# Optimization experiments

Measured on AMD Instinct MI355X. Metric: run time of the kernel, lower is better.

## Reference

```python
import jax, jax.numpy as jnp
import numpy as np

I_DIM = 512   # encoder feature size fed to CfC
UNITS = 1024  # AutoNCP total units (hidden_dim)
OUT = 128     # motor neurons (output_dim)
N = [538, 358, 128]                      # inter, command, motor layer sizes
IN_TOT = [I_DIM + N[0], N[0] + N[1], N[1] + N[2]]  # concat(input, h) width per layer
B, T = 512, 128


def setup_inputs() -> dict:
    key = jax.random.key(0)
    ks = jax.random.split(key, 40)
    d = {}
    d["x"] = jax.random.normal(ks[0], (B, T, I_DIM), jnp.float32)
    d["h0"] = jnp.zeros((B, UNITS), jnp.float32)
    ki = 1
    for l in range(3):
        it, n = IN_TOT[l], N[l]
        sp = (jax.random.uniform(ks[ki], (n, it - n)) < 0.5).astype(jnp.float32); ki += 1
        d[f"mask{l}"] = jnp.concatenate([sp, jnp.ones((n, n), jnp.float32)], axis=1)
        for name in ("Wff1", "Wff2", "Wta", "Wtb"):
            d[f"{name}_{l}"] = jax.random.normal(ks[ki], (n, it), jnp.float32) * float(1.0 / np.sqrt(it)); ki += 1
        for name in ("bff1", "bff2", "bta", "btb"):
            d[f"{name}_{l}"] = jnp.zeros((n,), jnp.float32)
    d["Wfc"] = jax.random.normal(ks[ki], (OUT, OUT), jnp.float32) * float(1.0 / np.sqrt(OUT))
    d["bfc"] = jnp.zeros((OUT,), jnp.float32)
    return d


def _cell(xin, h, p):
    # CfCCell, mode='default', no backbone, ts = 1.0
    W1, b1, W2, b2, Wa, ba, Wb, bb = p
    xc = jnp.concatenate([xin, h], axis=-1)           # (B, in+n)
    ff1 = jnp.tanh(xc @ W1.T + b1)
    ff2 = jnp.tanh(xc @ W2.T + b2)
    t_interp = jax.nn.sigmoid((xc @ Wa.T + ba) + (xc @ Wb.T + bb))
    return ff1 * (1.0 - t_interp) + t_interp * ff2


def reference(x, h0, mask0, Wff1_0, Wff2_0, Wta_0, Wtb_0, bff1_0, bff2_0, bta_0, btb_0,
              mask1, Wff1_1, Wff2_1, Wta_1, Wtb_1, bff1_1, bff2_1, bta_1, btb_1,
              mask2, Wff1_2, Wff2_2, Wta_2, Wtb_2, bff1_2, bff2_2, bta_2, btb_2,
              Wfc, bfc):
    params = (
        (Wff1_0 * mask0, bff1_0, Wff2_0 * mask0, bff2_0, Wta_0, bta_0, Wtb_0, btb_0),
        (Wff1_1 * mask1, bff1_1, Wff2_1 * mask1, bff2_1, Wta_1, bta_1, Wtb_1, btb_1),
        (Wff1_2 * mask2, bff1_2, Wff2_2 * mask2, bff2_2, Wta_2, bta_2, Wtb_2, btb_2),
    )
    hs0 = tuple(jnp.split(h0, [N[0], N[0] + N[1]], axis=1))

    def step(hs, x_t):
        inp = x_t
        new = []
        for l in range(3):
            inp = _cell(inp, hs[l], params[l])
            new.append(inp)
        return tuple(new), inp  # last layer (motor) is the cell output

    carry, outs = jax.lax.scan(step, hs0, jnp.swapaxes(x, 0, 1))
    outputs = jnp.swapaxes(outs, 0, 1)        # (B, T, OUT)
    hn = jnp.concatenate(carry, axis=1)       # (B, UNITS)
    predictions = outputs @ Wfc.T + bfc       # final nn.Linear
    return predictions, hn
```

## Files before the change

kernel.cpp:

```cpp
#include <hip/hip_runtime.h>
#include <stdint.h>

typedef __attribute__((ext_vector_type(8))) short short8;
typedef __attribute__((ext_vector_type(4))) float float4v;
typedef __attribute__((ext_vector_type(4))) unsigned short ushort4v;

constexpr int T = 128;
constexpr int NB = 512;
constexpr int NCH = 16;
constexpr int CBLK = 12;
constexpr int HS = 1056;

__device__ __forceinline__ float bf2f(ushort u) {
  union { float f; uint32_t i; } v; v.i = ((uint32_t)u) << 16; return v.f;
}
__device__ __forceinline__ ushort f2bf(float f) {
  union { float f; uint32_t i; } v; v.f = f;
  uint32_t i = v.i;
  uint32_t r = i + 0x7FFFu + ((i >> 16) & 1u);
  return (ushort)(r >> 16);
}

__device__ __forceinline__ unsigned long long coh_load8(const float* p) {
  return __hip_atomic_load(
      reinterpret_cast<unsigned long long*>(const_cast<float*>(p)),
      __ATOMIC_RELAXED, __HIP_MEMORY_SCOPE_AGENT);
}
__device__ __forceinline__ void coh_store8(float* p, float a, float b) {
  union { unsigned long long u; float f[2]; } v; v.f[0] = a; v.f[1] = b;
  __hip_atomic_store(reinterpret_cast<unsigned long long*>(p), v.u,
                     __ATOMIC_RELAXED, __HIP_MEMORY_SCOPE_AGENT);
}

__global__ __launch_bounds__(256) void pack_w(const float* __restrict__ W,
                                              const float* __restrict__ mask,
                                              ushort* __restrict__ out, int loOff,
                                              int NN, int IT, int NT, int KB,
                                              int POLD, int OLDLEN, int SOFF,
                                              int NEWLEN) {
  int idx = blockIdx.x * 256 + threadIdx.x;
  int total = KB * NT * 512;
  if (idx >= total) return;
  int jj   = idx & 7;
  int lane = (idx >> 3) & 63;
  int nt   = (idx >> 9) % NT;
  int kb   = (idx >> 9) / NT;
  int n = nt * 16 + (lane & 15);
  int p = kb * 32 + (lane >> 4) * 8 + jj;
  int src = -1;
  if (p < POLD) {
    if (p < OLDLEN) src = SOFF + p;
  } else {
    int q = p - POLD;
    if (q < NEWLEN) src = q;
  }
  float v = 0.f;
  if (n < NN && src >= 0) {
    v = W[(size_t)n * IT + src];
    if (mask) v *= mask[(size_t)n * IT + src];
  }
  ushort hi = f2bf(v);
  out[idx] = hi;
  out[loOff + idx] = f2bf(v - bf2f(hi));
}

template <int NTW, bool COH, int KB0, int KB1, int KOFF>
__device__ __forceinline__ void cell_range(
    ushort* __restrict__ Ast,
    const float* __restrict__ aRow,
    const ushort* __restrict__ wfq, int nt0, int NT, int loOff,
    float4v (&acc)[2][NTW]) {
  constexpr int PD = 4;
  constexpr int LEN = KB1 - KB0;
  constexpr int LEN2 = LEN & ~1;
  static_assert(LEN2 % PD == 0, "even part of every segment must be x4");
  const int tid  = threadIdx.x;
  const int lane = tid & 63, quad = lane >> 4, l16 = lane & 15;
  const int sm = tid >> 3;
  const int sk = (tid & 7) * 4;

  short8 cbh[PD][NTW], cbl[PD][NTW];
  float4v av[PD];

  auto loadB = [&](int kb, short8 (&bh)[NTW], short8 (&bl)[NTW]) {
#pragma unroll
    for (int w = 0; w < NTW; w++) {
      const size_t fo = ((size_t)(kb * NT + nt0 + w) * 64 + lane) * 8;
      bh[w] = *(const short8*)(wfq + fo);
      bl[w] = *(const short8*)(wfq + loOff + fo);
    }
  };
  auto loadA = [&](int kb) -> float4v {
    const float* p = aRow + (kb - KOFF) * 32 + sk;
    float4v r;
    if (COH) {
      union { unsigned long long u; float f[2]; } x0, x1;
      x0.u = coh_load8(p);
      x1.u = coh_load8(p + 2);
      r[0] = x0.f[0]; r[1] = x0.f[1]; r[2] = x1.f[0]; r[3] = x1.f[1];
    } else {
      r = *(const float4v*)p;
    }
    return r;
  };
  auto stageSlot = [&](int u, float4v a) {
    ushort4v hi4, lo4;
#pragma unroll
    for (int e = 0; e < 4; e++) {
      float v = a[e];
      ushort hi = f2bf(v);
      hi4[e] = hi;
      lo4[e] = f2bf(v - bf2f(hi));
    }
    *(ushort4v*)(Ast + u * 2560 + sm * 40 + sk) = hi4;
    *(ushort4v*)(Ast + u * 2560 + 1280 + sm * 40 + sk) = lo4;
  };
  auto mfmaSlot = [&](int u, const short8 (&bh)[NTW], const short8 (&bl)[NTW]) {
#pragma unroll
    for (int mt = 0; mt < 2; mt++) {
      short8 ah = *(const short8*)(Ast + u * 2560 + (mt * 16 + l16) * 40 + quad * 8);
      short8 al = *(const short8*)(Ast + u * 2560 + 1280 + (mt * 16 + l16) * 40 + quad * 8);
#pragma unroll
      for (int w = 0; w < NTW; w++) {
        acc[mt][w] = __builtin_amdgcn_mfma_f32_16x16x32_bf16(ah, bh[w], acc[mt][w], 0, 0, 0);
        acc[mt][w] = __builtin_amdgcn_mfma_f32_16x16x32_bf16(al, bh[w], acc[mt][w], 0, 0, 0);
        acc[mt][w] = __builtin_amdgcn_mfma_f32_16x16x32_bf16(ah, bl[w], acc[mt][w], 0, 0, 0);
      }
    }
  };

#pragma unroll
  for (int i = 0; i < PD; i++) { av[i] = loadA(KB0 + i); loadB(KB0 + i, cbh[i], cbl[i]); }

  for (int kb0 = KB0; kb0 < KB0 + LEN2; kb0 += PD) {
#pragma unroll
    for (int up = 0; up < 2; up++) {
      const int u0 = up * 2, u1 = up * 2 + 1;
      const int kb = kb0 + up * 2;
      stageSlot(u0, av[u0]);
      stageSlot(u1, av[u1]);
      asm volatile("s_waitcnt lgkmcnt(0)\n\ts_barrier" ::: "memory");
      mfmaSlot(u0, cbh[u0], cbl[u0]);
      mfmaSlot(u1, cbh[u1], cbl[u1]);
      if (kb + PD < KB1)     { av[u0] = loadA(kb + PD);     loadB(kb + PD,     cbh[u0], cbl[u0]); }
      if (kb + 1 + PD < KB1) { av[u1] = loadA(kb + 1 + PD); loadB(kb + 1 + PD, cbh[u1], cbl[u1]); }
    }
  }
  if (LEN & 1) {
    stageSlot(0, av[0]);
    asm volatile("s_waitcnt lgkmcnt(0)\n\ts_barrier" ::: "memory");
    mfmaSlot(0, cbh[0], cbl[0]);
  }
}

template <int NTW>
__device__ __forceinline__ void cell_epilogue(
    float* __restrict__ Acc, float4v (&acc)[2][NTW],
    const float* const* __restrict__ bias4,
    int NN, int NNPAD, float* __restrict__ hout, float* __restrict__ out2,
    int b0, int n0) {
  const int tid = threadIdx.x;
  const int wave = tid >> 6, lane = tid & 63, quad = lane >> 4, l16 = lane & 15;
  __syncthreads();
#pragma unroll
  for (int mt = 0; mt < 2; mt++)
#pragma unroll
    for (int w = 0; w < NTW; w++)
#pragma unroll
      for (int r = 0; r < 4; r++)
        Acc[(wave * 32 + mt * 16 + quad * 4 + r) * 50 + w * 16 + l16] = acc[mt][w][r];
  __syncthreads();
  constexpr int CW = 16 * NTW;
  for (int i4 = tid; i4 < 32 * (CW / 4); i4 += 256) {
    const int r = i4 / (CW / 4);
    const int c4 = (i4 % (CW / 4)) * 4;
    const int j0 = n0 + c4;
    if (j0 >= NNPAD) continue;
    float hv[4];
#pragma unroll
    for (int e = 0; e < 4; e++) {
      const int c = c4 + e, j = j0 + e;
      float h = 0.f;
      if (j < NN) {
        float v1 = Acc[(0 * 32 + r) * 50 + c] + bias4[0][j];
        float v2 = Acc[(1 * 32 + r) * 50 + c] + bias4[1][j];
        float va = Acc[(2 * 32 + r) * 50 + c] + bias4[2][j];
        float vb = Acc[(3 * 32 + r) * 50 + c] + bias4[3][j];
        float ff1 = tanhf(v1);
        float ff2 = tanhf(v2);
        float s = 1.f / (1.f + expf(-(va + vb)));
        h = ff1 * (1.f - s) + s * ff2;
      }
      hv[e] = h;
    }
    float* hp = hout + (size_t)(b0 + r) * HS + j0;
    coh_store8(hp, hv[0], hv[1]);
    coh_store8(hp + 2, hv[2], hv[3]);
    if (out2) {
      float4v o; o[0] = hv[0]; o[1] = hv[1]; o[2] = hv[2]; o[3] = hv[3];
      *(float4v*)(out2 + (size_t)(b0 + r) * 16384 + j0) = o;
    }
  }
}

struct PParams {
  const float* x;
  float* h0; float* h1;
  const ushort* wf0[4]; const ushort* wf1[4]; const ushort* wf2[4];
  int loOff0, loOff1, loOff2;
  const float* bias0[4]; const float* bias1[4]; const float* bias2[4];
  float* pred;
  int* bar;
};

__device__ __forceinline__ void bar_arrive(int* slot) {
  asm volatile("s_waitcnt vmcnt(0)" ::: "memory");
  __syncthreads();
  if (threadIdx.x == 0)
    __hip_atomic_fetch_add(slot, 1, __ATOMIC_RELAXED, __HIP_MEMORY_SCOPE_AGENT);
}
__device__ __forceinline__ void bar_wait(int* slot, int target) {
  if (threadIdx.x == 0) {
    while (__hip_atomic_load(slot, __ATOMIC_RELAXED, __HIP_MEMORY_SCOPE_AGENT) < target)
      __builtin_amdgcn_s_sleep(1);
  }
  __syncthreads();
}

__global__ __launch_bounds__(256, 1) void cfc_persistent(PParams p) {
  __shared__ ushort Ast[4 * 2560];
  __shared__ float  Acc[4 * 32 * 50];
  const int phys = blockIdx.x;
  const int s = (phys & 7) * 24 + (phys >> 3);
  const int ntp = s >> 4;
  const int c   = s & 15;
  const int b0 = c * 32;
  int* cbar = p.bar + c * (T * 3);
  const int wave = threadIdx.x >> 6;
  const int sm = threadIdx.x >> 3;
  const size_t rowoff = (size_t)(b0 + sm);

  for (int t = 0; t < T; t++) {
    float* hr = (t & 1) ? p.h1 : p.h0;
    float* hw = (t & 1) ? p.h0 : p.h1;
    const float* xRow  = p.x + rowoff * (T * 512) + (size_t)t * 512;
    const float* hrRow = hr + rowoff * HS;
    const float* hwRow = hw + rowoff * HS;

    float4v acc0[2][3];
#pragma unroll
    for (int i = 0; i < 2; i++)
#pragma unroll
      for (int w = 0; w < 3; w++) acc0[i][w] = float4v{0.f, 0.f, 0.f, 0.f};
    cell_range<3, false, 0, 16, 0 >(Ast, xRow,  p.wf0[wave], ntp * 3, 36, p.loOff0, acc0);
    cell_range<3, true, 16, 33, 16>(Ast, hrRow, p.wf0[wave], ntp * 3, 36, p.loOff0, acc0);
    cell_epilogue<3>(Acc, acc0, p.bias0, 538, 544, hw, nullptr, b0, ntp * 48);
    bar_arrive(cbar + t * 3);

    if (t && ntp >= 4) bar_wait(cbar + (t - 1) * 3 + 1, CBLK);
    float4v acc1[2][2];
#pragma unroll
    for (int i = 0; i < 2; i++)
#pragma unroll
      for (int w = 0; w < 2; w++) acc1[i][w] = float4v{0.f, 0.f, 0.f, 0.f};
    cell_range<2, true, 0, 12, 0 >(Ast, hrRow + 544, p.wf1[wave], ntp * 2, 24, p.loOff1, acc1);
    bar_wait(cbar + t * 3, CBLK);
    cell_range<2, true, 12, 29, 12>(Ast, hwRow, p.wf1[wave], ntp * 2, 24, p.loOff1, acc1);
    cell_epilogue<2>(Acc, acc1, p.bias1, 358, 384, hw + 544, nullptr, b0, ntp * 32);
    bar_arrive(cbar + t * 3 + 1);

    if (ntp < 4) {
      if (t) bar_wait(cbar + (t - 1) * 3 + 2, 4);
      float4v acc2[2][2];
#pragma unroll
      for (int i = 0; i < 2; i++)
#pragma unroll
        for (int w = 0; w < 2; w++) acc2[i][w] = float4v{0.f, 0.f, 0.f, 0.f};
      cell_range<2, true, 0, 4, 0>(Ast, hrRow + 928, p.wf2[wave], ntp * 2, 8, p.loOff2, acc2);
      bar_wait(cbar + t * 3 + 1, CBLK);
      cell_range<2, true, 4, 16, 4>(Ast, hwRow + 544, p.wf2[wave], ntp * 2, 8, p.loOff2, acc2);
      cell_epilogue<2>(Acc, acc2, p.bias2, 128, 128, hw + 928,
                       p.pred + (size_t)t * 128, b0, ntp * 32);
      bar_arrive(cbar + t * 3 + 2);
    }
  }
}

__global__ __launch_bounds__(256) void h_scatter(const float* __restrict__ src,
                                                 float* __restrict__ dst) {
  int idx = blockIdx.x * 256 + threadIdx.x;
  if (idx >= NB * HS) return;
  int b = idx / HS, u = idx % HS;
  int s = -1;
  if (u < 538) s = u;
  else if (u >= 544 && u < 902) s = 538 + (u - 544);
  else if (u >= 928) s = 896 + (u - 928);
  dst[idx] = (s >= 0) ? src[(size_t)b * 1024 + s] : 0.f;
}
__global__ __launch_bounds__(256) void h_gather(const float* __restrict__ src,
                                                float* __restrict__ dst) {
  int idx = blockIdx.x * 256 + threadIdx.x;
  if (idx >= NB * 1024) return;
  int b = idx / 1024, u = idx % 1024;
  int pu = (u < 538) ? u : (u < 896 ? (u - 538) + 544 : (u - 896) + 928);
  dst[idx] = src[(size_t)b * HS + pu];
}

__global__ __launch_bounds__(256)
void final_linear(float* __restrict__ io, const ushort* __restrict__ wfc_frag,
                  int loOff, const float* __restrict__ bfc) {
  __shared__ ushort Ah[64][136];
  __shared__ ushort Al[64][136];
  const int tid = threadIdx.x;
  const int wave = tid >> 6, lane = tid & 63, quad = lane >> 4, l16 = lane & 15;
  const size_t r0 = (size_t)blockIdx.x * 64;
  {
    const int row = tid >> 2;
    const int cb  = (tid & 3) * 32;
    const float* src = io + (r0 + row) * 128 + cb;
#pragma unroll
    for (int e = 0; e < 32; e++) {
      float v = src[e];
      ushort hi = f2bf(v);
      Ah[row][cb + e] = hi;
      Al[row][cb + e] = f2bf(v - bf2f(hi));
    }
  }
  __syncthreads();
  float4v acc[8];
#pragma unroll
  for (int i = 0; i < 8; i++) acc[i] = float4v{0.f, 0.f, 0.f, 0.f};
#pragma unroll
  for (int kb = 0; kb < 4; kb++) {
    short8 ah = *(const short8*)&Ah[wave * 16 + l16][kb * 32 + quad * 8];
    short8 al = *(const short8*)&Al[wave * 16 + l16][kb * 32 + quad * 8];
#pragma unroll
    for (int nt = 0; nt < 8; nt++) {
      const size_t fo = ((size_t)(kb * 8 + nt) * 64 + lane) * 8;
      short8 bh = *(const short8*)(wfc_frag + fo);
      short8 bl = *(const short8*)(wfc_frag + loOff + fo);
      acc[nt] = __builtin_amdgcn_mfma_f32_16x16x32_bf16(ah, bh, acc[nt], 0, 0, 0);
      acc[nt] = __builtin_amdgcn_mfma_f32_16x16x32_bf16(al, bh, acc[nt], 0, 0, 0);
      acc[nt] = __builtin_amdgcn_mfma_f32_16x16x32_bf16(ah, bl, acc[nt], 0, 0, 0);
    }
  }
  __syncthreads();
#pragma unroll
  for (int nt = 0; nt < 8; nt++) {
    int col = nt * 16 + l16;
    float bb = bfc[col];
#pragma unroll
    for (int r = 0; r < 4; r++) {
      int row = wave * 16 + quad * 4 + r;
      io[(r0 + row) * 128 + col] = acc[nt][r] + bb;
    }
  }
}

extern "C" void kernel_launch(void* const* d_in, const int* in_sizes, int n_in,
                              void* d_out, int out_size, void* d_ws, size_t ws_size,
                              hipStream_t stream) {
  const int maskIdx[3] = {2, 11, 20};
  const int wIdx[3]    = {3, 12, 21};
  const float* Wfc = (const float*)d_in[29];
  const float* bfc = (const float*)d_in[30];

  const int KBs[3]  = {33, 29, 16};
  const int NTs[3]  = {36, 24, 8};
  const int NNs[3]  = {538, 358, 128};
  const int ITs[3]  = {1050, 896, 486};
  const int POLDs[3]   = {0, 384, 128};
  const int OLDLENs[3] = {0, 358, 128};
  const int SOFFs[3]   = {0, 538, 358};
  const int NEWLENs[3] = {1050, 538, 358};

  ushort* ws = (ushort*)d_ws;
  size_t off = 0;
  ushort* wf[3][4];
  int loOff[3];
  for (int l = 0; l < 3; l++) {
    loOff[l] = KBs[l] * NTs[l] * 512;
    for (int q = 0; q < 4; q++) {
      wf[l][q] = ws + off;
      off += (size_t)2 * loOff[l];
    }
  }
  int wfcLo = 4 * 8 * 512;
  ushort* wfc_f = ws + off; off += (size_t)2 * wfcLo;
  float* hb0 = (float*)(ws + off); off += (size_t)NB * HS * 2;
  float* hb1 = (float*)(ws + off); off += (size_t)NB * HS * 2;
  int* bar = (int*)(ws + off); off += (size_t)NCH * T * 3 * 2;

  float* pred = (float*)d_out;
  float* hn   = (float*)d_out + (size_t)NB * T * 128;

  for (int l = 0; l < 3; l++) {
    int blocks = (loOff[l] + 255) / 256;
    for (int q = 0; q < 4; q++) {
      const float* m = (q < 2) ? (const float*)d_in[maskIdx[l]] : nullptr;
      pack_w<<<blocks, 256, 0, stream>>>((const float*)d_in[wIdx[l] + q], m, wf[l][q],
                                         loOff[l], NNs[l], ITs[l], NTs[l], KBs[l],
                                         POLDs[l], OLDLENs[l], SOFFs[l], NEWLENs[l]);
    }
  }
  pack_w<<<(wfcLo + 255) / 256, 256, 0, stream>>>(Wfc, nullptr, wfc_f, wfcLo,
                                                  128, 128, 8, 4, 0, 0, 0, 128);

  hipMemsetAsync(bar, 0, NCH * T * 3 * sizeof(int), stream);
  h_scatter<<<(NB * HS + 255) / 256, 256, 0, stream>>>((const float*)d_in[1], hb0);

  PParams p;
  p.x = (const float*)d_in[0];
  p.h0 = hb0; p.h1 = hb1;
  for (int q = 0; q < 4; q++) {
    p.wf0[q] = wf[0][q]; p.wf1[q] = wf[1][q]; p.wf2[q] = wf[2][q];
    p.bias0[q] = (const float*)d_in[7 + q];
    p.bias1[q] = (const float*)d_in[16 + q];
    p.bias2[q] = (const float*)d_in[25 + q];
  }
  p.loOff0 = loOff[0]; p.loOff1 = loOff[1]; p.loOff2 = loOff[2];
  p.pred = pred;
  p.bar = bar;

  cfc_persistent<<<NCH * CBLK, 256, 0, stream>>>(p);

  final_linear<<<(NB * T) / 64, 256, 0, stream>>>(pred, wfc_f, wfcLo, bfc);
  h_gather<<<(NB * 1024 + 255) / 256, 256, 0, stream>>>(hb0, hn);
}
```

Baseline: 5.749 ms.

## Halve rows per block to 16 and double block count with two blocks per CU

Changes the batch tile per block from 32 to 16 rows, giving 32 batch chunks instead of 16, so the persistent grid doubles to 384 blocks. Launch bounds now allow two blocks per CU. Staging, MFMA accumulators and the epilogue are resized to a single 16-row M tile. The goal is more parallel blocks to hide the latency of the recurrent chain, at the cost of reading each weight fragment twice as often per row and running more barriers.

```diff
diff --git a/kernel.cpp b/kernel.cpp
--- a/kernel.cpp
+++ b/kernel.cpp
@@ -3,11 +3,12 @@
 
 typedef __attribute__((ext_vector_type(8))) short short8;
 typedef __attribute__((ext_vector_type(4))) float float4v;
-typedef __attribute__((ext_vector_type(4))) unsigned short ushort4v;
+typedef __attribute__((ext_vector_type(2))) float float2v;
 
 constexpr int T = 128;
 constexpr int NB = 512;
-constexpr int NCH = 16;
+constexpr int NCH = 32;
+constexpr int ROWS = 16;
 constexpr int CBLK = 12;
 constexpr int HS = 1056;
 
@@ -69,68 +70,60 @@
     ushort* __restrict__ Ast,
     const float* __restrict__ aRow,
     const ushort* __restrict__ wfq, int nt0, int NT, int loOff,
-    float4v (&acc)[2][NTW]) {
+    float4v (&acc)[NTW]) {
   constexpr int PD = 4;
   constexpr int LEN = KB1 - KB0;
   constexpr int LEN2 = LEN & ~1;
-  static_assert(LEN2 % PD == 0, "even part of every segment must be x4");
+  static_assert(LEN2 % PD == 0 && KB0 % PD == 0, "slot mapping needs x4");
   const int tid  = threadIdx.x;
   const int lane = tid & 63, quad = lane >> 4, l16 = lane & 15;
-  const int sm = tid >> 3;
-  const int sk = (tid & 7) * 4;
+  const int sm = tid >> 4;
+  const int sk = (tid & 15) * 2;
 
   short8 cbh[PD][NTW], cbl[PD][NTW];
-  float4v av[PD];
-
-  auto loadB = [&](int kb, short8 (&bh)[NTW], short8 (&bl)[NTW]) {
+  float2v av[PD];
+
+  auto loadB = [&](int kb, int u) {
 #pragma unroll
     for (int w = 0; w < NTW; w++) {
       const size_t fo = ((size_t)(kb * NT + nt0 + w) * 64 + lane) * 8;
-      bh[w] = *(const short8*)(wfq + fo);
-      bl[w] = *(const short8*)(wfq + loOff + fo);
+      cbh[u][w] = *(const short8*)(wfq + fo);
+      cbl[u][w] = *(const short8*)(wfq + loOff + fo);
     }
   };
-  auto loadA = [&](int kb) -> float4v {
+  auto loadA = [&](int kb) -> float2v {
     const float* p = aRow + (kb - KOFF) * 32 + sk;
-    float4v r;
+    float2v r;
     if (COH) {
-      union { unsigned long long u; float f[2]; } x0, x1;
+      union { unsigned long long u; float f[2]; } x0;
       x0.u = coh_load8(p);
-      x1.u = coh_load8(p + 2);
-      r[0] = x0.f[0]; r[1] = x0.f[1]; r[2] = x1.f[0]; r[3] = x1.f[1];
+      r[0] = x0.f[0]; r[1] = x0.f[1];
     } else {
-      r = *(const float4v*)p;
+      r = *(const float2v*)p;
     }
     return r;
   };
-  auto stageSlot = [&](int u, float4v a) {
-    ushort4v hi4, lo4;
-#pragma unroll
-    for (int e = 0; e < 4; e++) {
-      float v = a[e];
-      ushort hi = f2bf(v);
-      hi4[e] = hi;
-      lo4[e] = f2bf(v - bf2f(hi));
-    }
-    *(ushort4v*)(Ast + u * 2560 + sm * 40 + sk) = hi4;
-    *(ushort4v*)(Ast + u * 2560 + 1280 + sm * 40 + sk) = lo4;
+  auto stageSlot = [&](int u, float2v a) {
+    ushort h0 = f2bf(a[0]), h1 = f2bf(a[1]);
+    ushort l0 = f2bf(a[0] - bf2f(h0)), l1 = f2bf(a[1] - bf2f(h1));
+    uint32_t hp = (uint32_t)h0 | ((uint32_t)h1 << 16);
+    uint32_t lp = (uint32_t)l0 | ((uint32_t)l1 << 16);
+    *(uint32_t*)(Ast + u * 1280 + sm * 40 + sk) = hp;
+    *(uint32_t*)(Ast + u * 1280 + 640 + sm * 40 + sk) = lp;
   };
   auto mfmaSlot = [&](int u, const short8 (&bh)[NTW], const short8 (&bl)[NTW]) {
-#pragma unroll
-    for (int mt = 0; mt < 2; mt++) {
-      short8 ah = *(const short8*)(Ast + u * 2560 + (mt * 16 + l16) * 40 + quad * 8);
-      short8 al = *(const short8*)(Ast + u * 2560 + 1280 + (mt * 16 + l16) * 40 + quad * 8);
-#pragma unroll
-      for (int w = 0; w < NTW; w++) {
-        acc[mt][w] = __builtin_amdgcn_mfma_f32_16x16x32_bf16(ah, bh[w], acc[mt][w], 0, 0, 0);
-        acc[mt][w] = __builtin_amdgcn_mfma_f32_16x16x32_bf16(al, bh[w], acc[mt][w], 0, 0, 0);
-        acc[mt][w] = __builtin_amdgcn_mfma_f32_16x16x32_bf16(ah, bl[w], acc[mt][w], 0, 0, 0);
-      }
+    short8 ah = *(const short8*)(Ast + u * 1280 + l16 * 40 + quad * 8);
+    short8 al = *(const short8*)(Ast + u * 1280 + 640 + l16 * 40 + quad * 8);
+#pragma unroll
+    for (int w = 0; w < NTW; w++) {
+      acc[w] = __builtin_amdgcn_mfma_f32_16x16x32_bf16(ah, bh[w], acc[w], 0, 0, 0);
+      acc[w] = __builtin_amdgcn_mfma_f32_16x16x32_bf16(al, bh[w], acc[w], 0, 0, 0);
+      acc[w] = __builtin_amdgcn_mfma_f32_16x16x32_bf16(ah, bl[w], acc[w], 0, 0, 0);
     }
   };
 
 #pragma unroll
-  for (int i = 0; i < PD; i++) { av[i] = loadA(KB0 + i); loadB(KB0 + i, cbh[i], cbl[i]); }
+  for (int i = 0; i < PD; i++) { av[i] = loadA(KB0 + i); loadB(KB0 + i, i); }
 
   for (int kb0 = KB0; kb0 < KB0 + LEN2; kb0 += PD) {
 #pragma unroll
@@ -142,8 +135,8 @@
       asm volatile("s_waitcnt lgkmcnt(0)\n\ts_barrier" ::: "memory");
       mfmaSlot(u0, cbh[u0], cbl[u0]);
       mfmaSlot(u1, cbh[u1], cbl[u1]);
-      if (kb + PD < KB1)     { av[u0] = loadA(kb + PD);     loadB(kb + PD,     cbh[u0], cbl[u0]); }
-      if (kb + 1 + PD < KB1) { av[u1] = loadA(kb + 1 + PD); loadB(kb + 1 + PD, cbh[u1], cbl[u1]); }
+      if (kb + PD < KB1)     { av[u0] = loadA(kb + PD);     loadB(kb + PD,     u0); }
+      if (kb + 1 + PD < KB1) { av[u1] = loadA(kb + 1 + PD); loadB(kb + 1 + PD, u1); }
     }
   }
   if (LEN & 1) {
@@ -155,7 +148,7 @@
 
 template <int NTW>
 __device__ __forceinline__ void cell_epilogue(
-    float* __restrict__ Acc, float4v (&acc)[2][NTW],
+    float* __restrict__ Acc, float4v (&acc)[NTW],
     const float* const* __restrict__ bias4,
     int NN, int NNPAD, float* __restrict__ hout, float* __restrict__ out2,
     int b0, int n0) {
@@ -163,15 +156,13 @@
   const int wave = tid >> 6, lane = tid & 63, quad = lane >> 4, l16 = lane & 15;
   __syncthreads();
 #pragma unroll
-  for (int mt = 0; mt < 2; mt++)
-#pragma unroll
-    for (int w = 0; w < NTW; w++)
-#pragma unroll
-      for (int r = 0; r < 4; r++)
-        Acc[(wave * 32 + mt * 16 + quad * 4 + r) * 50 + w * 16 + l16] = acc[mt][w][r];
+  for (int w = 0; w < NTW; w++)
+#pragma unroll
+    for (int r = 0; r < 4; r++)
+      Acc[(wave * 16 + quad * 4 + r) * 50 + w * 16 + l16] = acc[w][r];
   __syncthreads();
   constexpr int CW = 16 * NTW;
-  for (int i4 = tid; i4 < 32 * (CW / 4); i4 += 256) {
+  for (int i4 = tid; i4 < 16 * (CW / 4); i4 += 256) {
     const int r = i4 / (CW / 4);
     const int c4 = (i4 % (CW / 4)) * 4;
     const int j0 = n0 + c4;
@@ -182,10 +173,10 @@
       const int c = c4 + e, j = j0 + e;
       float h = 0.f;
       if (j < NN) {
-        float v1 = Acc[(0 * 32 + r) * 50 + c] + bias4[0][j];
-        float v2 = Acc[(1 * 32 + r) * 50 + c] + bias4[1][j];
-        float va = Acc[(2 * 32 + r) * 50 + c] + bias4[2][j];
-        float vb = Acc[(3 * 32 + r) * 50 + c] + bias4[3][j];
+        float v1 = Acc[(0 * 16 + r) * 50 + c] + bias4[0][j];
+        float v2 = Acc[(1 * 16 + r) * 50 + c] + bias4[1][j];
+        float va = Acc[(2 * 16 + r) * 50 + c] + bias4[2][j];
+        float vb = Acc[(3 * 16 + r) * 50 + c] + bias4[3][j];
         float ff1 = tanhf(v1);
         float ff2 = tanhf(v2);
         float s = 1.f / (1.f + expf(-(va + vb)));
@@ -227,18 +218,21 @@
   __syncthreads();
 }
 
-__global__ __launch_bounds__(256, 1) void cfc_persistent(PParams p) {
-  __shared__ ushort Ast[4 * 2560];
-  __shared__ float  Acc[4 * 32 * 50];
+__global__ __launch_bounds__(256, 2) void cfc_persistent(PParams p) {
+  __shared__ ushort Ast[4 * 1280];
+  __shared__ float  Acc[4 * 16 * 50];
   const int phys = blockIdx.x;
-  const int s = (phys & 7) * 24 + (phys >> 3);
-  const int ntp = s >> 4;
-  const int c   = s & 15;
-  const int b0 = c * 32;
+  const int s = (phys & 7) * 48 + (phys >> 3);
+  const int ntp = s >> 5;
+  const int c   = s & 31;
+  const int b0 = c * ROWS;
   int* cbar = p.bar + c * (T * 3);
   const int wave = threadIdx.x >> 6;
-  const int sm = threadIdx.x >> 3;
+  const int sm = threadIdx.x >> 4;
   const size_t rowoff = (size_t)(b0 + sm);
+  const ushort* wq0 = p.wf0[wave];
+  const ushort* wq1 = p.wf1[wave];
+  const ushort* wq2 = p.wf2[wave];
 
   for (int t = 0; t < T; t++) {
     float* hr = (t & 1) ? p.h1 : p.h0;
@@ -247,38 +241,32 @@
     const float* hrRow = hr + rowoff * HS;
     const float* hwRow = hw + rowoff * HS;
 
-    float4v acc0[2][3];
-#pragma unroll
-    for (int i = 0; i < 2; i++)
-#pragma unroll
-      for (int w = 0; w < 3; w++) acc0[i][w] = float4v{0.f, 0.f, 0.f, 0.f};
-    cell_range<3, false, 0, 16, 0 >(Ast, xRow,  p.wf0[wave], ntp * 3, 36, p.loOff0, acc0);
-    cell_range<3, true, 16, 33, 16>(Ast, hrRow, p.wf0[wave], ntp * 3, 36, p.loOff0, acc0);
+    float4v acc0[3];
+#pragma unroll
+    for (int w = 0; w < 3; w++) acc0[w] = float4v{0.f, 0.f, 0.f, 0.f};
+    cell_range<3, false, 0, 16, 0 >(Ast, xRow,  wq0, ntp * 3, 36, p.loOff0, acc0);
+    cell_range<3, true, 16, 33, 16>(Ast, hrRow, wq0, ntp * 3, 36, p.loOff0, acc0);
     cell_epilogue<3>(Acc, acc0, p.bias0, 538, 544, hw, nullptr, b0, ntp * 48);
     bar_arrive(cbar + t * 3);
 
     if (t && ntp >= 4) bar_wait(cbar + (t - 1) * 3 + 1, CBLK);
-    float4v acc1[2][2];
-#pragma unroll
-    for (int i = 0; i < 2; i++)
-#pragma unroll
-      for (int w = 0; w < 2; w++) acc1[i][w] = float4v{0.f, 0.f, 0.f, 0.f};
-    cell_range<2, true, 0, 12, 0 >(Ast, hrRow + 544, p.wf1[wave], ntp * 2, 24, p.loOff1, acc1);
+    float4v acc1[2];
+#pragma unroll
+    for (int w = 0; w < 2; w++) acc1[w] = float4v{0.f, 0.f, 0.f, 0.f};
+    cell_range<2, true, 0, 12, 0 >(Ast, hrRow + 544, wq1, ntp * 2, 24, p.loOff1, acc1);
     bar_wait(cbar + t * 3, CBLK);
-    cell_range<2, true, 12, 29, 12>(Ast, hwRow, p.wf1[wave], ntp * 2, 24, p.loOff1, acc1);
+    cell_range<2, true, 12, 29, 12>(Ast, hwRow, wq1, ntp * 2, 24, p.loOff1, acc1);
     cell_epilogue<2>(Acc, acc1, p.bias1, 358, 384, hw + 544, nullptr, b0, ntp * 32);
     bar_arrive(cbar + t * 3 + 1);
 
     if (ntp < 4) {
       if (t) bar_wait(cbar + (t - 1) * 3 + 2, 4);
-      float4v acc2[2][2];
-#pragma unroll
-      for (int i = 0; i < 2; i++)
-#pragma unroll
-        for (int w = 0; w < 2; w++) acc2[i][w] = float4v{0.f, 0.f, 0.f, 0.f};
-      cell_range<2, true, 0, 4, 0>(Ast, hrRow + 928, p.wf2[wave], ntp * 2, 8, p.loOff2, acc2);
+      float4v acc2[2];
+#pragma unroll
+      for (int w = 0; w < 2; w++) acc2[w] = float4v{0.f, 0.f, 0.f, 0.f};
+      cell_range<2, true, 0, 4, 0>(Ast, hrRow + 928, wq2, ntp * 2, 8, p.loOff2, acc2);
       bar_wait(cbar + t * 3 + 1, CBLK);
-      cell_range<2, true, 4, 16, 4>(Ast, hwRow + 544, p.wf2[wave], ntp * 2, 8, p.loOff2, acc2);
+      cell_range<2, true, 4, 16, 4>(Ast, hwRow + 544, wq2, ntp * 2, 8, p.loOff2, acc2);
       cell_epilogue<2>(Acc, acc2, p.bias2, 128, 128, hw + 928,
                        p.pred + (size_t)t * 128, b0, ntp * 32);
       bar_arrive(cbar + t * 3 + 2);
```

After: 22.87 ms. +297.8%, slower.
